# Kernel optimization log

Hardware: AMD Instinct MI355X
Metric: run time of the kernel (lower is better)

## Reference

```python
import math
import jax, jax.numpy as jnp
import numpy as np

EMBED_DIM = 2048
NUM_HEADS = 16
HEAD_DIM = EMBED_DIM // NUM_HEADS
CHUNK = 128
RMS_EPS = 1e-5


def _build_slopes(n):
    # ALiBi-style slopes (power-of-2 branch; n=16 is a power of 2)
    def pow2(n):
        start = 2.0 ** (-(2.0 ** -(math.log2(n) - 3)))
        return [start * (start ** i) for i in range(n)]
    if math.log2(n).is_integer():
        s = pow2(n)
    else:
        closest = 2 ** math.floor(math.log2(n))
        s = pow2(closest) + pow2(2 * closest)[0::2][: n - closest]
    return jnp.asarray(s, dtype=jnp.float32)


def _rotary(x_BTHD, offset=0):
    # x: [B, T, H, D]; D//4 nonzero freqs + D//4 zero freqs -> D//2 angles
    T, D = x_BTHD.shape[1], x_BTHD.shape[-1]
    freq = (1.0 / 1024.0) ** jnp.linspace(0.0, 1.0, D // 4, dtype=jnp.float32)
    freq = jnp.concatenate([freq, jnp.zeros(D // 4, dtype=jnp.float32)])
    t = jnp.arange(offset, offset + T, dtype=jnp.float32)
    theta = t[:, None] * freq[None, :]            # [T, D/2]
    cos = jnp.cos(theta)[None, :, None, :]
    sin = jnp.sin(theta)[None, :, None, :]
    x1, x2 = jnp.split(x_BTHD.astype(jnp.float32), 2, axis=-1)
    y1 = x1 * cos + x2 * sin
    y2 = -x1 * sin + x2 * cos
    return jnp.concatenate([y1, y2], axis=-1).astype(x_BTHD.dtype)


def _lightning_attn(q, k, v, slopes):
    # q,k,v: [B, H, T, D]; decayed causal linear attention:
    #   o_t = q_t @ sum_{s<=t} exp(-slope*(t-s)) * k_s v_s^T
    B, H, T, D = q.shape
    C = CHUNK
    NC = T // C
    r = jnp.exp(-slopes)                          # [H]
    i = jnp.arange(C, dtype=jnp.float32)
    # factors within a chunk
    q_decay = r[:, None] ** (i[None, :] + 1.0)    # [H, C] : r^{i+1}
    k_decay = r[:, None] ** (C - 1.0 - i[None, :])  # [H, C] : r^{C-1-i}
    diff = i[:, None] - i[None, :]                # t - s
    mask = diff >= 0
    dmask = jnp.where(mask[None], r[:, None, None] ** jnp.where(mask, diff, 0.0)[None], 0.0)  # [H,C,C]
    r_C = r ** float(C)                            # [H]

    def reshape_chunks(x):
        return x.reshape(B, H, NC, C, D).transpose(2, 0, 1, 3, 4)  # [NC,B,H,C,D]

    qc, kc, vc = reshape_chunks(q), reshape_chunks(k), reshape_chunks(v)

    def step(kv, qkv):
        qi, ki, vi = qkv                          # [B,H,C,D]
        inter = jnp.einsum('bhcd,bhde->bhce', qi * q_decay[None, :, :, None], kv)
        scores = jnp.einsum('bhcd,bhsd->bhcs', qi, ki) * dmask[None]
        intra = jnp.einsum('bhcs,bhse->bhce', scores, vi)
        kv_new = r_C[None, :, None, None] * kv + jnp.einsum(
            'bhcd,bhce->bhde', ki * k_decay[None, :, :, None], vi)
        return kv_new, inter + intra

    kv0 = jnp.zeros((B, H, D, D), dtype=q.dtype)
    _, out = jax.lax.scan(step, kv0, (qc, kc, vc))  # [NC,B,H,C,D]
    return out.transpose(1, 2, 0, 3, 4).reshape(B, H, T, D)


def _rms_norm(x, w):
    var = jnp.mean(jnp.square(x), axis=-1, keepdims=True)
    return x * jax.lax.rsqrt(var + RMS_EPS) * w


def setup_inputs() -> dict:
    key = jax.random.key(0)
    ks = jax.random.split(key, 6)
    sc = 1.0 / math.sqrt(EMBED_DIM)
    return {
        'x': jax.random.normal(ks[0], (4, 4096, EMBED_DIM), dtype=jnp.float32),
        'Wq': jax.random.normal(ks[1], (EMBED_DIM, EMBED_DIM), dtype=jnp.float32) * sc,
        'Wk': jax.random.normal(ks[2], (EMBED_DIM, EMBED_DIM), dtype=jnp.float32) * sc,
        'Wv': jax.random.normal(ks[3], (EMBED_DIM, EMBED_DIM), dtype=jnp.float32) * sc,
        'Wo': jax.random.normal(ks[4], (EMBED_DIM, EMBED_DIM), dtype=jnp.float32) * sc,
        'rms_w': jnp.ones((EMBED_DIM,), dtype=jnp.float32),
    }


def reference(x, Wq, Wk, Wv, Wo, rms_w):
    B, T, E = x.shape
    H, D = NUM_HEADS, HEAD_DIM
    q = (x @ Wq).reshape(B, T, H, D)
    k = (x @ Wk).reshape(B, T, H, D)
    v = (x @ Wv).reshape(B, T, H, D)
    q = _rotary(q)
    k = _rotary(k)
    q, k, v = (t.transpose(0, 2, 1, 3) for t in (q, k, v))  # [B,H,T,D]
    slopes = _build_slopes(H)
    attn = _lightning_attn(q, k, v, slopes)       # [B,H,T,D]
    attn = attn.transpose(0, 2, 1, 3).reshape(B, T, E)
    attn = _rms_norm(attn, rms_w)
    return attn @ Wo
```

## Files before the change

### kernel.cpp

```cpp
#include <hip/hip_runtime.h>

typedef unsigned short ushort;
typedef float f32x4 __attribute__((ext_vector_type(4)));
typedef __bf16 bf16x8 __attribute__((ext_vector_type(8)));
typedef ushort u16x4 __attribute__((ext_vector_type(4)));
typedef ushort u16x8 __attribute__((ext_vector_type(8)));

#define LOG2E 1.4426950408889634f

__device__ __forceinline__ ushort f2bu(float f) { __bf16 b = (__bf16)f; return __builtin_bit_cast(ushort, b); }
__device__ __forceinline__ float  bu2f(ushort u) { return (float)__builtin_bit_cast(__bf16, u); }

__device__ __forceinline__ void gld16(const void* g, void* l) {
    __builtin_amdgcn_global_load_lds((const __attribute__((address_space(1))) unsigned int*)g,
                                     (__attribute__((address_space(3))) unsigned int*)l, 16, 0, 0);
}

__global__ __launch_bounds__(256) void k_cvt(const float* __restrict__ in, ushort* __restrict__ out, int n4) {
    int i = blockIdx.x * 256 + threadIdx.x;
    if (i < n4) {
        float4 v = ((const float4*)in)[i];
        u16x4 o = { f2bu(v.x), f2bu(v.y), f2bu(v.z), f2bu(v.w) };
        ((u16x4*)out)[i] = o;
    }
}

__global__ __launch_bounds__(256) void k_twt(const float* __restrict__ W, ushort* __restrict__ Wt) {
    __shared__ float t[32][33];
    int n0 = blockIdx.x * 32, k0 = blockIdx.y * 32;
    int tx = threadIdx.x & 31, ty = threadIdx.x >> 5;
#pragma unroll
    for (int i = 0; i < 32; i += 8) t[ty + i][tx] = W[(size_t)(k0 + ty + i) * 2048 + n0 + tx];
    __syncthreads();
#pragma unroll
    for (int i = 0; i < 32; i += 8) Wt[(size_t)(n0 + ty + i) * 2048 + k0 + tx] = f2bu(t[tx][ty + i]);
}

__global__ __launch_bounds__(256) void k_rope(float* __restrict__ tab) {
    int idx = blockIdx.x * 256 + threadIdx.x;
    int t = idx >> 5, j = idx & 31;
    float fr = exp2f(-10.0f * (float)j / 31.0f);
    float th = (float)t * fr;
    tab[idx * 2]     = cosf(th);
    tab[idx * 2 + 1] = sinf(th);
}

#define AOFF(buf, kh) ((buf) * 32768 + (kh) * 16384)
#define BOFF(buf, kh) (65536 + (buf) * 32768 + (kh) * 16384)

#define STG_A(BUFX, KHX, KKX) do {                                                 \
    gld16(asrc0 + ((KKX) + (KHX) * 32) * 2, lds + AOFF(BUFX, KHX) + ldst);         \
    gld16(asrc1 + ((KKX) + (KHX) * 32) * 2, lds + AOFF(BUFX, KHX) + 8192 + ldst);  \
} while (0)
#define STG_B(BUFX, KHX, KKX) do {                                                 \
    gld16(bsrc0 + ((KKX) + (KHX) * 32) * 2, lds + BOFF(BUFX, KHX) + ldst);         \
    gld16(bsrc1 + ((KKX) + (KHX) * 32) * 2, lds + BOFF(BUFX, KHX) + 8192 + ldst);  \
} while (0)

#define PHASE(BUF, KH, MH, LDB, STAGE_STMT, TAILVM) do {                           \
    bf16x8 af_[4];                                                                 \
    const char* ab_ = lds + AOFF(BUF, KH);                                         \
    _Pragma("unroll")                                                              \
    for (int mi_ = 0; mi_ < 4; ++mi_)                                              \
        af_[mi_] = *(const bf16x8*)(ab_ + offA[(MH) * 4 + mi_]);                   \
    if (LDB) {                                                                     \
        const char* bb_ = lds + BOFF(BUF, KH);                                     \
        _Pragma("unroll")                                                          \
        for (int ni_ = 0; ni_ < 4; ++ni_)                                          \
            bfr[ni_] = *(const bf16x8*)(bb_ + offB[ni_]);                          \
    }                                                                              \
    STAGE_STMT;                                                                    \
    __builtin_amdgcn_s_barrier();                                                  \
    asm volatile("s_waitcnt lgkmcnt(0)" ::: "memory");                             \
    __builtin_amdgcn_sched_barrier(0);                                             \
    __builtin_amdgcn_s_setprio(1);                                                 \
    _Pragma("unroll")                                                              \
    for (int mi_ = 0; mi_ < 4; ++mi_)                                              \
        _Pragma("unroll")                                                          \
        for (int ni_ = 0; ni_ < 4; ++ni_)                                          \
            acc[(MH) * 4 + mi_][ni_] = __builtin_amdgcn_mfma_f32_16x16x32_bf16(    \
                af_[mi_], bfr[ni_], acc[(MH) * 4 + mi_][ni_], 0, 0, 0);            \
    __builtin_amdgcn_s_setprio(0);                                                 \
    TAILVM;                                                                        \
    __builtin_amdgcn_s_barrier();                                                  \
} while (0)

#define TILE(BUF, TC) do {                                                         \
    int tp1_ = (TC) + 1 < 32 ? (TC) + 1 : 31;                                      \
    int tp2_ = (TC) + 2 < 32 ? (TC) + 2 : 31;                                      \
    int kb1_ = tp1_ * 64, kb2_ = tp2_ * 64;                                        \
    PHASE(BUF, 0, 0, 1, STG_A((BUF) ^ 1, 1, kb1_), ((void)0));                     \
    PHASE(BUF, 0, 1, 0, STG_B((BUF) ^ 1, 1, kb1_),                                 \
          asm volatile("s_waitcnt vmcnt(8)" ::: "memory"));                        \
    PHASE(BUF, 1, 0, 1, STG_A(BUF, 0, kb2_), ((void)0));                           \
    PHASE(BUF, 1, 1, 0, STG_B(BUF, 0, kb2_),                                       \
          asm volatile("s_waitcnt vmcnt(8)" ::: "memory"));                        \
} while (0)

template <int OUTF32, int NPX>
__global__ __launch_bounds__(512, 2) void k_gemm(const ushort* __restrict__ A, const ushort* __restrict__ Bt,
                                                 float* __restrict__ Cf, ushort* __restrict__ C0,
                                                 ushort* __restrict__ C1, ushort* __restrict__ C2) {
    __shared__ __align__(128) char lds[131072];
    const int tid = threadIdx.x;
    const int wid = tid >> 6, lane = tid & 63;
    const int wm = wid >> 2, wn = wid & 3;
    const int lrow = lane & 15, q = lane >> 4;

    int bid = blockIdx.x;
    int xcd = bid & 7, local = bid >> 3;
    int nloc = local % NPX, mloc = local / NPX;
    size_t n0 = (size_t)(xcd * NPX + nloc) * 256;
    size_t m0 = (size_t)mloc * 256;

    int offA[8], offB[4];
#pragma unroll
    for (int mi = 0; mi < 8; ++mi) {
        int R = wm * 128 + mi * 16 + lrow;
        offA[mi] = R * 64 + ((q ^ ((R >> 1) & 3)) << 4);
    }
#pragma unroll
    for (int ni = 0; ni < 4; ++ni) {
        int R = wn * 64 + ni * 16 + lrow;
        offB[ni] = R * 64 + ((q ^ ((R >> 1) & 3)) << 4);
    }

    int srow0 = tid >> 2;
    int cw = (tid & 3) ^ ((tid >> 3) & 3);
    const char* asrc0 = (const char*)(A + (m0 + srow0) * 2048 + cw * 8);
    const char* asrc1 = (const char*)(A + (m0 + srow0 + 128) * 2048 + cw * 8);
    const char* bsrc0 = (const char*)(Bt + (n0 + srow0) * 2048 + cw * 8);
    const char* bsrc1 = (const char*)(Bt + (n0 + srow0 + 128) * 2048 + cw * 8);
    const int ldst = tid * 16;

    f32x4 acc[8][4] = {};
    bf16x8 bfr[4];

    STG_A(0, 0, 0); STG_B(0, 0, 0); STG_A(0, 1, 0); STG_B(0, 1, 0);
    STG_A(1, 0, 64); STG_B(1, 0, 64);
    asm volatile("s_waitcnt vmcnt(8)" ::: "memory");
    __builtin_amdgcn_s_barrier();

#pragma unroll 1
    for (int t = 0; t < 32; t += 2) {
        TILE(0, t);
        TILE(1, t + 1);
    }

    int tsel = (int)(n0 >> 11);
    size_t ncol = n0 & 2047;
    ushort* Cb = (tsel == 0) ? C0 : ((tsel == 1) ? C1 : C2);
#pragma unroll
    for (int mi = 0; mi < 8; ++mi)
#pragma unroll
        for (int ni = 0; ni < 4; ++ni)
#pragma unroll
            for (int i = 0; i < 4; ++i) {
                size_t row = m0 + wm * 128 + mi * 16 + (lane >> 4) * 4 + i;
                size_t col = wn * 64 + ni * 16 + lrow;
                if (OUTF32) Cf[row * 2048 + n0 + col] = acc[mi][ni][i];
                else        Cb[row * 2048 + ncol + col] = f2bu(acc[mi][ni][i]);
            }
}

__global__ __launch_bounds__(256) void k_reshape(const ushort* __restrict__ Cin, ushort* __restrict__ outN,
                                                 ushort* __restrict__ outT, const float* __restrict__ rt, int mode) {
    int blk = blockIdx.x;
    int c = blk & 31, bh = blk >> 5, b = bh >> 4, h = bh & 15;
    __shared__ __align__(16) ushort lt[128][136];
    int tid = threadIdx.x;
    int d = tid & 63, rq = tid >> 6;
    float slope = exp2f(-0.5f * (float)(h + 1));
    float l2r = -slope * LOG2E;
    for (int rp = 0; rp < 32; ++rp) {
        int tr = rp * 4 + rq;
        int t = c * 128 + tr;
        const ushort* src = Cin + ((size_t)(b * 4096 + t)) * 2048 + h * 128;
        float x1 = bu2f(src[d]), x2 = bu2f(src[d + 64]);
        float y1 = x1, y2 = x2;
        if (mode != 2 && d < 32) {
            float cs = rt[(t * 32 + d) * 2], sn = rt[(t * 32 + d) * 2 + 1];
            y1 = x1 * cs + x2 * sn;
            y2 = x2 * cs - x1 * sn;
        }
        if (mode != 2) {
            ushort* dstN = outN + ((size_t)bh * 4096 + t) * 128;
            dstN[d] = f2bu(y1); dstN[d + 64] = f2bu(y2);
        }
        if (mode != 0) { lt[tr][d] = f2bu(y1); lt[tr][d + 64] = f2bu(y2); }
    }
    if (mode == 0) return;
    __syncthreads();
    int dd = tid >> 1, half = tid & 1;
    ushort* dstT = outT + ((size_t)bh * 128 + dd) * 4096 + c * 128 + half * 64;
    for (int j8 = 0; j8 < 8; ++j8) {
        u16x8 tmp;
#pragma unroll
        for (int j = 0; j < 8; ++j) {
            int s = half * 64 + j8 * 8 + j;
            float v = bu2f(lt[s][dd]);
            if (mode == 1) v *= exp2f(l2r * (float)(127 - s));
            tmp[j] = f2bu(v);
        }
        *(u16x8*)(dstT + j8 * 8) = tmp;
    }
}

__global__ __launch_bounds__(256) void k_pass1(const ushort* __restrict__ kTa, const ushort* __restrict__ vTa,
                                               float* __restrict__ KVc) {
    int blk = blockIdx.x;
    int c = blk & 31, bh = blk >> 5;
    __shared__ __align__(16) ushort lv[128][136];
    __shared__ __align__(16) ushort lk[128][136];
    int tid = threadIdx.x;
#pragma unroll
    for (int i = 0; i < 8; ++i) {
        int idx = i * 256 + tid; int row = idx >> 4, cb = (idx & 15) * 8;
        *(bf16x8*)&lv[row][cb] = *(const bf16x8*)(vTa + ((size_t)bh * 128 + row) * 4096 + c * 128 + cb);
        *(bf16x8*)&lk[row][cb] = *(const bf16x8*)(kTa + ((size_t)bh * 128 + row) * 4096 + c * 128 + cb);
    }
    __syncthreads();
    int wid = tid >> 6, lane = tid & 63, wr = wid >> 1, wc = wid & 1;
    int lrow = lane & 15, lko = (lane >> 4) * 8;
    f32x4 acc[4][4] = {};
#pragma unroll
    for (int ks = 0; ks < 4; ++ks) {
        bf16x8 a[4], bb[4];
#pragma unroll
        for (int mi = 0; mi < 4; ++mi) a[mi] = *(const bf16x8*)&lv[wr * 64 + mi * 16 + lrow][ks * 32 + lko];
#pragma unroll
        for (int ni = 0; ni < 4; ++ni) bb[ni] = *(const bf16x8*)&lk[wc * 64 + ni * 16 + lrow][ks * 32 + lko];
#pragma unroll
        for (int mi = 0; mi < 4; ++mi)
#pragma unroll
            for (int ni = 0; ni < 4; ++ni)
                acc[mi][ni] = __builtin_amdgcn_mfma_f32_16x16x32_bf16(a[mi], bb[ni], acc[mi][ni], 0, 0, 0);
    }
    float* out = KVc + (size_t)blk * 16384;
#pragma unroll
    for (int mi = 0; mi < 4; ++mi)
#pragma unroll
        for (int ni = 0; ni < 4; ++ni)
#pragma unroll
            for (int i = 0; i < 4; ++i)
                out[(wr * 64 + mi * 16 + (lane >> 4) * 4 + i) * 128 + wc * 64 + ni * 16 + lrow] = acc[mi][ni][i];
}

__global__ __launch_bounds__(256) void k_scan(const float* __restrict__ KVc, ushort* __restrict__ KVbf) {
    int bh = blockIdx.x >> 4, seg = blockIdx.x & 15, h = bh & 15;
    float slope = exp2f(-0.5f * (float)(h + 1));
    float rC = exp2f(-slope * LOG2E * 128.0f);
    int off = seg * 1024 + threadIdx.x * 4;
    f32x4 st = {0.f, 0.f, 0.f, 0.f};
    for (int c = 0; c < 32; ++c) {
        size_t base = ((size_t)bh * 32 + c) * 16384 + off;
        f32x4 v = *(const f32x4*)(KVc + base);
        u16x4 o = { f2bu(st.x), f2bu(st.y), f2bu(st.z), f2bu(st.w) };
        *(u16x4*)(KVbf + base) = o;
        st = st * rC + v;
    }
}

__global__ __launch_bounds__(512) void k_pass3(const ushort* __restrict__ qa, const ushort* __restrict__ ka,
                                               const ushort* __restrict__ vTa, const ushort* __restrict__ KVbf,
                                               ushort* __restrict__ attn) {
    int blk = blockIdx.x;
    int c = blk & 31, bh = blk >> 5, h = bh & 15;
    __shared__ __align__(16) ushort lq[128][136];
    __shared__ __align__(16) ushort lk[128][136];
    __shared__ __align__(16) ushort lv[128][136];
    int tid = threadIdx.x;
#pragma unroll
    for (int i = 0; i < 4; ++i) {
        int idx = i * 512 + tid; int row = idx >> 4, cb = (idx & 15) * 8;
        *(bf16x8*)&lq[row][cb] = *(const bf16x8*)(qa + ((size_t)bh * 4096 + c * 128 + row) * 128 + cb);
        *(bf16x8*)&lk[row][cb] = *(const bf16x8*)(ka + ((size_t)bh * 4096 + c * 128 + row) * 128 + cb);
        *(bf16x8*)&lv[row][cb] = *(const bf16x8*)(vTa + ((size_t)bh * 128 + row) * 4096 + c * 128 + cb);
    }
    __syncthreads();
    int wid = tid >> 6, lane = tid & 63;
    int wr = wid >> 2, wc = wid & 3;
    int lrow = lane & 15, lko = (lane >> 4) * 8;
    float slope = exp2f(-0.5f * (float)(h + 1));
    float l2r = -slope * LOG2E;

    f32x4 accs[4][2] = {};
#pragma unroll
    for (int kd = 0; kd < 4; ++kd) {
        bf16x8 a[4], bb[2];
#pragma unroll
        for (int mi = 0; mi < 4; ++mi) a[mi] = *(const bf16x8*)&lq[wr * 64 + mi * 16 + lrow][kd * 32 + lko];
#pragma unroll
        for (int ni = 0; ni < 2; ++ni) bb[ni] = *(const bf16x8*)&lk[wc * 32 + ni * 16 + lrow][kd * 32 + lko];
#pragma unroll
        for (int mi = 0; mi < 4; ++mi)
#pragma unroll
            for (int ni = 0; ni < 2; ++ni)
                accs[mi][ni] = __builtin_amdgcn_mfma_f32_16x16x32_bf16(a[mi], bb[ni], accs[mi][ni], 0, 0, 0);
    }
    __syncthreads();

    f32x4 acc[4][2] = {};
#pragma unroll
    for (int kd = 0; kd < 4; ++kd) {
        bf16x8 a[4], bb[2];
#pragma unroll
        for (int mi = 0; mi < 4; ++mi) a[mi] = *(const bf16x8*)&lq[wr * 64 + mi * 16 + lrow][kd * 32 + lko];
#pragma unroll
        for (int ni = 0; ni < 2; ++ni)
            bb[ni] = *(const bf16x8*)(KVbf + (size_t)blk * 16384 + (size_t)(wc * 32 + ni * 16 + lrow) * 128 + kd * 32 + lko);
#pragma unroll
        for (int mi = 0; mi < 4; ++mi)
#pragma unroll
            for (int ni = 0; ni < 2; ++ni)
                acc[mi][ni] = __builtin_amdgcn_mfma_f32_16x16x32_bf16(a[mi], bb[ni], acc[mi][ni], 0, 0, 0);
    }

#pragma unroll
    for (int mi = 0; mi < 4; ++mi)
#pragma unroll
        for (int ni = 0; ni < 2; ++ni)
#pragma unroll
            for (int i = 0; i < 4; ++i) {
                int t = wr * 64 + mi * 16 + (lane >> 4) * 4 + i;
                int s = wc * 32 + ni * 16 + lrow;
                int dt = t - s;
                float w = (dt < 0) ? 0.f : exp2f(l2r * (float)dt);
                lk[t][s] = f2bu(accs[mi][ni][i] * w);
            }

#pragma unroll
    for (int mi = 0; mi < 4; ++mi)
#pragma unroll
        for (int ni = 0; ni < 2; ++ni)
#pragma unroll
            for (int i = 0; i < 4; ++i) {
                int t = wr * 64 + mi * 16 + (lane >> 4) * 4 + i;
                acc[mi][ni][i] *= exp2f(l2r * (float)(t + 1));
            }
    __syncthreads();

#pragma unroll
    for (int ks = 0; ks < 4; ++ks) {
        bf16x8 a[4], bb[2];
#pragma unroll
        for (int mi = 0; mi < 4; ++mi) a[mi] = *(const bf16x8*)&lk[wr * 64 + mi * 16 + lrow][ks * 32 + lko];
#pragma unroll
        for (int ni = 0; ni < 2; ++ni) bb[ni] = *(const bf16x8*)&lv[wc * 32 + ni * 16 + lrow][ks * 32 + lko];
#pragma unroll
        for (int mi = 0; mi < 4; ++mi)
#pragma unroll
            for (int ni = 0; ni < 2; ++ni)
                acc[mi][ni] = __builtin_amdgcn_mfma_f32_16x16x32_bf16(a[mi], bb[ni], acc[mi][ni], 0, 0, 0);
    }

    ushort* out = attn + ((size_t)bh * 4096 + c * 128) * 128;
#pragma unroll
    for (int mi = 0; mi < 4; ++mi)
#pragma unroll
        for (int ni = 0; ni < 2; ++ni)
#pragma unroll
            for (int i = 0; i < 4; ++i)
                out[(size_t)(wr * 64 + mi * 16 + (lane >> 4) * 4 + i) * 128 + wc * 32 + ni * 16 + lrow] =
                    f2bu(acc[mi][ni][i]);
}

__global__ __launch_bounds__(256) void k_rms(const ushort* __restrict__ attn, const float* __restrict__ w,
                                             ushort* __restrict__ normed) {
    int tok = blockIdx.x; int b = tok >> 12, t = tok & 4095;
    int tid = threadIdx.x;
    int e0 = tid * 8; int h = e0 >> 7, d0 = e0 & 127;
    bf16x8 v = *(const bf16x8*)(attn + (((size_t)(b * 16 + h) * 4096 + t) * 128 + d0));
    float f[8]; float ss = 0.f;
#pragma unroll
    for (int j = 0; j < 8; ++j) { f[j] = (float)v[j]; ss += f[j] * f[j]; }
#pragma unroll
    for (int o = 1; o < 64; o <<= 1) ss += __shfl_xor(ss, o, 64);
    __shared__ float red[4];
    if ((tid & 63) == 0) red[tid >> 6] = ss;
    __syncthreads();
    float tot = red[0] + red[1] + red[2] + red[3];
    float sc = rsqrtf(tot * (1.0f / 2048.0f) + 1e-5f);
    u16x8 ov;
#pragma unroll
    for (int j = 0; j < 8; ++j) ov[j] = f2bu(f[j] * sc * w[e0 + j]);
    *(u16x8*)(normed + (size_t)tok * 2048 + e0) = ov;
}

extern "C" void kernel_launch(void* const* d_in, const int* in_sizes, int n_in,
                              void* d_out, int out_size, void* d_ws, size_t ws_size,
                              hipStream_t stream) {
    const float* x    = (const float*)d_in[0];
    const float* Wq   = (const float*)d_in[1];
    const float* Wk   = (const float*)d_in[2];
    const float* Wv   = (const float*)d_in[3];
    const float* Wo   = (const float*)d_in[4];
    const float* rmsw = (const float*)d_in[5];
    char* ws = (char*)d_ws;
    const size_t MiB = 1ull << 20;
    ushort* WtQKV = (ushort*)(ws + 0);
    ushort* WtK   = (ushort*)(ws + 8 * MiB);
    ushort* WtV   = (ushort*)(ws + 16 * MiB);
    ushort* WtO   = (ushort*)(ws + 24 * MiB);
    ushort* xb    = (ushort*)(ws + 32 * MiB);
    ushort* CQ    = (ushort*)(ws + 96 * MiB);
    ushort* CK    = (ushort*)(ws + 160 * MiB);
    ushort* CV    = (ushort*)(ws + 224 * MiB);
    ushort* qa    = (ushort*)(ws + 288 * MiB);
    ushort* ka    = (ushort*)(ws + 352 * MiB);
    float*  rt    = (float*)(ws + 416 * MiB);
    ushort* kTa   = (ushort*)(ws + 32 * MiB);
    ushort* vTa   = (ushort*)(ws + 96 * MiB);
    float*  KVc   = (float*)(ws + 160 * MiB);
    ushort* KVbf  = (ushort*)(ws + 32 * MiB);
    ushort* attn  = (ushort*)(ws + 224 * MiB);
    ushort* nrm   = (ushort*)(ws + 96 * MiB);

    k_cvt<<<32768, 256, 0, stream>>>(x, xb, 8388608);
    dim3 gw(64, 64);
    k_twt<<<gw, 256, 0, stream>>>(Wq, WtQKV);
    k_twt<<<gw, 256, 0, stream>>>(Wk, WtK);
    k_twt<<<gw, 256, 0, stream>>>(Wv, WtV);
    k_twt<<<gw, 256, 0, stream>>>(Wo, WtO);
    k_rope<<<512, 256, 0, stream>>>(rt);

    k_gemm<0, 3><<<1536, 512, 0, stream>>>(xb, WtQKV, nullptr, CQ, CK, CV);
    k_reshape<<<2048, 256, 0, stream>>>(CQ, qa, nullptr, rt, 0);
    k_reshape<<<2048, 256, 0, stream>>>(CK, ka, kTa, rt, 1);
    k_reshape<<<2048, 256, 0, stream>>>(CV, nullptr, vTa, rt, 2);

    k_pass1<<<2048, 256, 0, stream>>>(kTa, vTa, KVc);
    k_scan<<<1024, 256, 0, stream>>>(KVc, KVbf);
    k_pass3<<<2048, 512, 0, stream>>>(qa, ka, vTa, KVbf, attn);

    k_rms<<<16384, 256, 0, stream>>>(attn, rmsw, nrm);
    k_gemm<1, 1><<<512, 512, 0, stream>>>(nrm, WtO, (float*)d_out, nullptr, nullptr, nullptr);
}
```

Measured before the change: 994.9 us.

## Fuse rotary, head reshape and K/V transposes into QKV GEMM epilogue

The QKV projection GEMM now stages its output tile through LDS and writes the rotary-applied head-major q/k directly, plus the decay-scaled transposed k and the transposed v. This removes the three separate reshape kernels and the round trip of the bf16 CQ/CK/CV intermediates through global memory. The workspace is reorganised, with the KV chunk buffer split into two halves, and the output GEMM tile mapping is changed. In exchange the GEMM epilogue becomes longer, adds several block barriers, and issues uncoalesced rope-table reads.

Result: slower. 1.365 ms (+37.2%).

```diff
diff --git a/kernel.cpp b/kernel.cpp
--- a/kernel.cpp
+++ b/kernel.cpp
@@ -97,10 +97,11 @@
           asm volatile("s_waitcnt vmcnt(8)" ::: "memory"));                        \
 } while (0)
 
-template <int OUTF32, int NPX>
+template <int MODE>
 __global__ __launch_bounds__(512, 2) void k_gemm(const ushort* __restrict__ A, const ushort* __restrict__ Bt,
-                                                 float* __restrict__ Cf, ushort* __restrict__ C0,
-                                                 ushort* __restrict__ C1, ushort* __restrict__ C2) {
+                                                 const float* __restrict__ rt, float* __restrict__ Cf,
+                                                 ushort* __restrict__ qa, ushort* __restrict__ ka,
+                                                 ushort* __restrict__ kTa, ushort* __restrict__ vTa) {
     __shared__ __align__(128) char lds[131072];
     const int tid = threadIdx.x;
     const int wid = tid >> 6, lane = tid & 63;
@@ -109,9 +110,11 @@
 
     int bid = blockIdx.x;
     int xcd = bid & 7, local = bid >> 3;
-    int nloc = local % NPX, mloc = local / NPX;
-    size_t n0 = (size_t)(xcd * NPX + nloc) * 256;
-    size_t m0 = (size_t)mloc * 256;
+    int nt, mloc;
+    if (MODE == 0) { nt = xcd + (local % 3) * 8; mloc = local / 3; }
+    else           { nt = local & 7;             mloc = xcd * 8 + (local >> 3); }
+    const size_t n0 = (size_t)nt * 256;
+    const size_t m0 = (size_t)mloc * 256;
 
     int offA[8], offB[4];
 #pragma unroll
@@ -147,67 +150,109 @@
         TILE(1, t + 1);
     }
 
-    int tsel = (int)(n0 >> 11);
-    size_t ncol = n0 & 2047;
-    ushort* Cb = (tsel == 0) ? C0 : ((tsel == 1) ? C1 : C2);
-#pragma unroll
-    for (int mi = 0; mi < 8; ++mi)
-#pragma unroll
-        for (int ni = 0; ni < 4; ++ni)
-#pragma unroll
-            for (int i = 0; i < 4; ++i) {
-                size_t row = m0 + wm * 128 + mi * 16 + (lane >> 4) * 4 + i;
-                size_t col = wn * 64 + ni * 16 + lrow;
-                if (OUTF32) Cf[row * 2048 + n0 + col] = acc[mi][ni][i];
-                else        Cb[row * 2048 + ncol + col] = f2bu(acc[mi][ni][i]);
+    if (MODE == 1) {
+#pragma unroll
+        for (int mi = 0; mi < 8; ++mi)
+#pragma unroll
+            for (int ni = 0; ni < 4; ++ni)
+#pragma unroll
+                for (int i = 0; i < 4; ++i) {
+                    size_t row = m0 + wm * 128 + mi * 16 + q * 4 + i;
+                    size_t col = n0 + wn * 64 + ni * 16 + lrow;
+                    Cf[row * 2048 + col] = acc[mi][ni][i];
+                }
+        return;
+    }
+
+    asm volatile("s_waitcnt vmcnt(0)" ::: "memory");
+    __syncthreads();
+    ushort* ldsu = (ushort*)lds;
+    const int tsel = nt >> 3;
+    const int b = (int)(m0 >> 12);
+    const int tseq0 = (int)(m0 & 4095);
+    const int hbase = ((int)(n0 & 2047)) >> 7;
+
+    for (int st = 0; st < 2; ++st) {
+        if (wm == st) {
+#pragma unroll
+            for (int mi = 0; mi < 8; ++mi)
+#pragma unroll
+                for (int ni = 0; ni < 4; ++ni)
+#pragma unroll
+                    for (int i = 0; i < 4; ++i) {
+                        int r = mi * 16 + q * 4 + i;
+                        int cc = wn * 64 + ni * 16 + lrow;
+                        ldsu[((r * 512 + cc * 2) ^ ((r & 7) << 4)) >> 1] = f2bu(acc[mi][ni][i]);
+                    }
+        }
+        __syncthreads();
+        if (tsel != 2) {
+            int rowid = tid >> 1, half = tid & 1;
+            int hl = rowid >> 7, r = rowid & 127;
+            int t = tseq0 + st * 128 + r;
+            int bh = b * 16 + hbase + hl;
+            ushort* dstN = (tsel == 0 ? qa : ka) + ((size_t)bh * 4096 + t) * 128;
+            int rx = (r & 7) << 4;
+#pragma unroll
+            for (int j8 = 0; j8 < 4; ++j8) {
+                if (half == 0) {
+                    int b1 = ((r * 512 + (hl * 128 + j8 * 8) * 2) ^ rx) >> 1;
+                    int b2 = ((r * 512 + (hl * 128 + 64 + j8 * 8) * 2) ^ rx) >> 1;
+                    u16x8 v1 = *(u16x8*)&ldsu[b1];
+                    u16x8 v2 = *(u16x8*)&ldsu[b2];
+                    u16x8 o1, o2;
+#pragma unroll
+                    for (int j = 0; j < 8; ++j) {
+                        int d = j8 * 8 + j;
+                        float cs = rt[(t * 32 + d) * 2], sn = rt[(t * 32 + d) * 2 + 1];
+                        float x1 = bu2f(v1[j]), x2 = bu2f(v2[j]);
+                        o1[j] = f2bu(x1 * cs + x2 * sn);
+                        o2[j] = f2bu(x2 * cs - x1 * sn);
+                    }
+                    *(u16x8*)(dstN + j8 * 8) = o1;
+                    *(u16x8*)(dstN + 64 + j8 * 8) = o2;
+                    if (tsel == 1) {
+                        *(u16x8*)&ldsu[b1] = o1;
+                        *(u16x8*)&ldsu[b2] = o2;
+                    }
+                } else {
+                    int b1 = ((r * 512 + (hl * 128 + 32 + j8 * 8) * 2) ^ rx) >> 1;
+                    int b2 = ((r * 512 + (hl * 128 + 96 + j8 * 8) * 2) ^ rx) >> 1;
+                    u16x8 v1 = *(u16x8*)&ldsu[b1];
+                    u16x8 v2 = *(u16x8*)&ldsu[b2];
+                    *(u16x8*)(dstN + 32 + j8 * 8) = v1;
+                    *(u16x8*)(dstN + 96 + j8 * 8) = v2;
+                }
             }
-}
-
-__global__ __launch_bounds__(256) void k_reshape(const ushort* __restrict__ Cin, ushort* __restrict__ outN,
-                                                 ushort* __restrict__ outT, const float* __restrict__ rt, int mode) {
-    int blk = blockIdx.x;
-    int c = blk & 31, bh = blk >> 5, b = bh >> 4, h = bh & 15;
-    __shared__ __align__(16) ushort lt[128][136];
-    int tid = threadIdx.x;
-    int d = tid & 63, rq = tid >> 6;
-    float slope = exp2f(-0.5f * (float)(h + 1));
-    float l2r = -slope * LOG2E;
-    for (int rp = 0; rp < 32; ++rp) {
-        int tr = rp * 4 + rq;
-        int t = c * 128 + tr;
-        const ushort* src = Cin + ((size_t)(b * 4096 + t)) * 2048 + h * 128;
-        float x1 = bu2f(src[d]), x2 = bu2f(src[d + 64]);
-        float y1 = x1, y2 = x2;
-        if (mode != 2 && d < 32) {
-            float cs = rt[(t * 32 + d) * 2], sn = rt[(t * 32 + d) * 2 + 1];
-            y1 = x1 * cs + x2 * sn;
-            y2 = x2 * cs - x1 * sn;
         }
-        if (mode != 2) {
-            ushort* dstN = outN + ((size_t)bh * 4096 + t) * 128;
-            dstN[d] = f2bu(y1); dstN[d + 64] = f2bu(y2);
+        if (tsel != 0) {
+            __syncthreads();
+            int drow = tid >> 1, th = tid & 1;
+            int hl = drow >> 7, d = drow & 127;
+            int bh = b * 16 + hbase + hl;
+            float l2r = -exp2f(-0.5f * (float)(hbase + hl + 1)) * LOG2E;
+            int t0 = tseq0 + st * 128;
+            ushort* dstT = (tsel == 1 ? kTa : vTa) + ((size_t)bh * 128 + d) * 4096 + t0 + th * 64;
+#pragma unroll
+            for (int g = 0; g < 8; ++g) {
+                u16x8 tmp;
+#pragma unroll
+                for (int j = 0; j < 8; ++j) {
+                    int rr = th * 64 + g * 8 + j;
+                    int idx = ((rr * 512 + (hl * 128 + d) * 2) ^ ((rr & 7) << 4)) >> 1;
+                    float v = bu2f(ldsu[idx]);
+                    if (tsel == 1) v *= exp2f(l2r * (float)(127 - rr));
+                    tmp[j] = f2bu(v);
+                }
+                *(u16x8*)(dstT + g * 8) = tmp;
+            }
         }
-        if (mode != 0) { lt[tr][d] = f2bu(y1); lt[tr][d + 64] = f2bu(y2); }
-    }
-    if (mode == 0) return;
-    __syncthreads();
-    int dd = tid >> 1, half = tid & 1;
-    ushort* dstT = outT + ((size_t)bh * 128 + dd) * 4096 + c * 128 + half * 64;
-    for (int j8 = 0; j8 < 8; ++j8) {
-        u16x8 tmp;
-#pragma unroll
-        for (int j = 0; j < 8; ++j) {
-            int s = half * 64 + j8 * 8 + j;
-            float v = bu2f(lt[s][dd]);
-            if (mode == 1) v *= exp2f(l2r * (float)(127 - s));
-            tmp[j] = f2bu(v);
-        }
-        *(u16x8*)(dstT + j8 * 8) = tmp;
+        __syncthreads();
     }
 }
 
 __global__ __launch_bounds__(256) void k_pass1(const ushort* __restrict__ kTa, const ushort* __restrict__ vTa,
-                                               float* __restrict__ KVc) {
+                                               float* __restrict__ KVlo, float* __restrict__ KVhi) {
     int blk = blockIdx.x;
     int c = blk & 31, bh = blk >> 5;
     __shared__ __align__(16) ushort lv[128][136];
@@ -236,7 +281,7 @@
             for (int ni = 0; ni < 4; ++ni)
                 acc[mi][ni] = __builtin_amdgcn_mfma_f32_16x16x32_bf16(a[mi], bb[ni], acc[mi][ni], 0, 0, 0);
     }
-    float* out = KVc + (size_t)blk * 16384;
+    float* out = (bh < 32) ? (KVlo + (size_t)blk * 16384) : (KVhi + (size_t)(blk - 1024) * 16384);
 #pragma unroll
     for (int mi = 0; mi < 4; ++mi)
 #pragma unroll
@@ -246,17 +291,18 @@
                 out[(wr * 64 + mi * 16 + (lane >> 4) * 4 + i) * 128 + wc * 64 + ni * 16 + lrow] = acc[mi][ni][i];
 }
 
-__global__ __launch_bounds__(256) void k_scan(const float* __restrict__ KVc, ushort* __restrict__ KVbf) {
+__global__ __launch_bounds__(256) void k_scan(const float* __restrict__ KVlo, const float* __restrict__ KVhi,
+                                              ushort* __restrict__ KVbf) {
     int bh = blockIdx.x >> 4, seg = blockIdx.x & 15, h = bh & 15;
     float slope = exp2f(-0.5f * (float)(h + 1));
     float rC = exp2f(-slope * LOG2E * 128.0f);
     int off = seg * 1024 + threadIdx.x * 4;
+    const float* base = (bh < 32) ? (KVlo + (size_t)bh * 32 * 16384) : (KVhi + (size_t)(bh - 32) * 32 * 16384);
     f32x4 st = {0.f, 0.f, 0.f, 0.f};
     for (int c = 0; c < 32; ++c) {
-        size_t base = ((size_t)bh * 32 + c) * 16384 + off;
-        f32x4 v = *(const f32x4*)(KVc + base);
+        f32x4 v = *(const f32x4*)(base + (size_t)c * 16384 + off);
         u16x4 o = { f2bu(st.x), f2bu(st.y), f2bu(st.z), f2bu(st.w) };
-        *(u16x4*)(KVbf + base) = o;
+        *(u16x4*)(KVbf + ((size_t)bh * 32 + c) * 16384 + off) = o;
         st = st * rC + v;
     }
 }
@@ -403,17 +449,15 @@
     ushort* WtV   = (ushort*)(ws + 16 * MiB);
     ushort* WtO   = (ushort*)(ws + 24 * MiB);
     ushort* xb    = (ushort*)(ws + 32 * MiB);
-    ushort* CQ    = (ushort*)(ws + 96 * MiB);
-    ushort* CK    = (ushort*)(ws + 160 * MiB);
-    ushort* CV    = (ushort*)(ws + 224 * MiB);
-    ushort* qa    = (ushort*)(ws + 288 * MiB);
-    ushort* ka    = (ushort*)(ws + 352 * MiB);
-    float*  rt    = (float*)(ws + 416 * MiB);
-    ushort* kTa   = (ushort*)(ws + 32 * MiB);
-    ushort* vTa   = (ushort*)(ws + 96 * MiB);
-    float*  KVc   = (float*)(ws + 160 * MiB);
-    ushort* KVbf  = (ushort*)(ws + 32 * MiB);
-    ushort* attn  = (ushort*)(ws + 224 * MiB);
+    ushort* qa    = (ushort*)(ws + 96 * MiB);
+    ushort* ka    = (ushort*)(ws + 160 * MiB);
+    ushort* kTa   = (ushort*)(ws + 224 * MiB);
+    ushort* vTa   = (ushort*)(ws + 288 * MiB);
+    float*  rt    = (float*)(ws + 352 * MiB);
+    float*  KVlo  = (float*)(ws + 32 * MiB);
+    float*  KVhi  = (float*)(ws + 353 * MiB);
+    ushort* KVbf  = (ushort*)(ws + 224 * MiB);
+    ushort* attn  = (ushort*)(ws + 32 * MiB);
     ushort* nrm   = (ushort*)(ws + 96 * MiB);
 
     k_cvt<<<32768, 256, 0, stream>>>(x, xb, 8388608);
@@ -424,15 +468,12 @@
     k_twt<<<gw, 256, 0, stream>>>(Wo, WtO);
     k_rope<<<512, 256, 0, stream>>>(rt);
 
-    k_gemm<0, 3><<<1536, 512, 0, stream>>>(xb, WtQKV, nullptr, CQ, CK, CV);
-    k_reshape<<<2048, 256, 0, stream>>>(CQ, qa, nullptr, rt, 0);
-    k_reshape<<<2048, 256, 0, stream>>>(CK, ka, kTa, rt, 1);
-    k_reshape<<<2048, 256, 0, stream>>>(CV, nullptr, vTa, rt, 2);
-
-    k_pass1<<<2048, 256, 0, stream>>>(kTa, vTa, KVc);
-    k_scan<<<1024, 256, 0, stream>>>(KVc, KVbf);
+    k_gemm<0><<<1536, 512, 0, stream>>>(xb, WtQKV, rt, nullptr, qa, ka, kTa, vTa);
+
+    k_pass1<<<2048, 256, 0, stream>>>(kTa, vTa, KVlo, KVhi);
+    k_scan<<<1024, 256, 0, stream>>>(KVlo, KVhi, KVbf);
     k_pass3<<<2048, 512, 0, stream>>>(qa, ka, vTa, KVbf, attn);
 
     k_rms<<<16384, 256, 0, stream>>>(attn, rmsw, nrm);
-    k_gemm<1, 1><<<512, 512, 0, stream>>>(nrm, WtO, (float*)d_out, nullptr, nullptr, nullptr);
-}
+    k_gemm<1><<<512, 512, 0, stream>>>(nrm, WtO, nullptr, (float*)d_out, nullptr, nullptr, nullptr, nullptr);
+}
```
